# Kernel tuning notes

Measured on AMD Instinct MI355X. Metric: run time of the kernel, lower is better.

## Reference

```python
import jax, jax.numpy as jnp
import numpy as np

B, CIN, T, H, W = 4, 3, 32, 64, 64
COUT = 64


def setup_inputs() -> dict:
    key = jax.random.key(0)
    ks = jax.random.split(key, 6)
    X = jax.random.normal(ks[0], (B, CIN, T, H, W), jnp.float32)
    # Conv3d weight (O, I, D, kH, kW) for kernel (2,3,3)
    Wconv = jax.random.normal(ks[1], (4 * COUT, CIN, 2, 3, 3), jnp.float32) * 0.1
    bconv = jax.random.normal(ks[2], (4 * COUT,), jnp.float32) * 0.1
    # QRNNCell peephole params, shape (out_channels, *frame_size)
    W_ci = jax.random.normal(ks[3], (COUT, H, W), jnp.float32) * 0.1
    W_cf = jax.random.normal(ks[4], (COUT, H, W), jnp.float32) * 0.1
    W_co = jax.random.normal(ks[5], (COUT, H, W), jnp.float32) * 0.1
    return {"X": X, "Wconv": Wconv, "bconv": bconv,
            "W_ci": W_ci, "W_cf": W_cf, "W_co": W_co}


def reference(X, Wconv, bconv, W_ci, W_cf, W_co):
    # ConstantPad3d((1,1,1,1,1,0)): W +-1, H +-1, time front +1
    Xp = jnp.pad(X, ((0, 0), (0, 0), (1, 0), (1, 1), (1, 1)))
    # Conv3d, kernel (2,3,3), VALID -> output (B, 4*COUT, T, H, W)
    E = jax.lax.conv_general_dilated(
        Xp, Wconv, window_strides=(1, 1, 1), padding='VALID',
        dimension_numbers=('NCDHW', 'OIDHW', 'NCDHW'))
    E = E + bconv[None, :, None, None, None]
    i_c, f_c, g_c, o_c = jnp.split(E, 4, axis=1)  # each (B, COUT, T, H, W)
    # time-major stacked gates: (T, 4, B, COUT, H, W)
    gates = jnp.stack([jnp.moveaxis(x, 2, 0) for x in (i_c, f_c, g_c, o_c)], axis=1)

    def step(carry, g4):
        Hs, Cs = carry
        i, f, g, o = g4[0], g4[1], g4[2], g4[3]
        ig = jax.nn.sigmoid(i + W_ci * Cs)
        fg = jax.nn.sigmoid(f + W_cf * Cs)
        Cn = fg * Cs + ig * jnp.tanh(g)
        og = jax.nn.sigmoid(o + W_co * Cn)
        Hn = og * jnp.tanh(Cn)
        return (Hn, Cn), Hn

    z = jnp.zeros((X.shape[0], W_ci.shape[0], X.shape[3], X.shape[4]), X.dtype)
    _, outs = jax.lax.scan(step, (z, z), gates)  # outs: (T, B, COUT, H, W)
    return jnp.moveaxis(outs, 0, 2)  # (B, COUT, T, H, W)
```

## Files before the change

kernel.cpp:

```cpp
#include <hip/hip_runtime.h>

#define TT     32
#define HW     4096
#define LROW   68
#define LPLANE (6 * LROW)
#define SXSZ   (3 * LPLANE)
#define NSTG   (3 * 6 * 66)

__device__ __forceinline__ float fsigmoid(float x) {
    return __builtin_amdgcn_rcpf(1.0f + __builtin_amdgcn_exp2f(x * -1.4426950408889634f));
}
__device__ __forceinline__ float ftanh(float x) {
    return 2.0f * __builtin_amdgcn_rcpf(1.0f + __builtin_amdgcn_exp2f(x * -2.8853900817779268f)) - 1.0f;
}
__device__ __forceinline__ float sgprf(float v) {
    return __uint_as_float(__builtin_amdgcn_readfirstlane(__float_as_uint(v)));
}

__global__ __launch_bounds__(256, 2) void convqrnn(
    const float* __restrict__ X,
    const float* __restrict__ Wc,
    const float* __restrict__ bc,
    const float* __restrict__ Wci,
    const float* __restrict__ Wcf,
    const float* __restrict__ Wco,
    float* __restrict__ out)
{
    __shared__ float sx[2 * SXSZ];
    __shared__ float gb[2 * 2048];
    __shared__ float wl[576];

    const int tid = threadIdx.x;
    const int h0  = blockIdx.x * 4;
    const int co0 = blockIdx.y * 2;
    const int b   = blockIdx.z;

    const int g  = tid >> 6;
    const int l  = tid & 63;
    const int r  = l >> 4;
    const int c0 = (l & 15) * 4;

    const int prow = tid >> 6;
    const int pcol = tid & 63;
    const int opix = (h0 + prow) * 64 + pcol;

    const float wciA = Wci[co0 * HW + opix];
    const float wcfA = Wcf[co0 * HW + opix];
    const float wcoA = Wco[co0 * HW + opix];
    const float wciB = Wci[(co0 + 1) * HW + opix];
    const float wcfB = Wcf[(co0 + 1) * HW + opix];
    const float wcoB = Wco[(co0 + 1) * HW + opix];

    for (int fi = tid; fi < 432; fi += 256) {
        int grp   = fi / 12;
        int e     = fi - grp * 12;
        int g2    = grp / 9;
        int ck    = grp - g2 * 9;
        int ci    = ck / 3;
        int kh    = ck - ci * 3;
        int which = e / 3;
        int kw    = e - which * 3;
        int cs    = which >> 1;
        int dt    = which & 1;
        wl[grp * 16 + e] =
            Wc[(size_t)(g2 * 64 + co0 + cs) * 54 + ci * 18 + dt * 9 + kh * 3 + kw];
    }
    const float bgA = sgprf(bc[g * 64 + co0]);
    const float bgB = sgprf(bc[g * 64 + co0 + 1]);

    const float* __restrict__ Xb = X + (size_t)b * (3 * TT * HW);
    int soff[5];
    int goff[5];
    int svmask = 0;
    #pragma unroll
    for (int k = 0; k < 5; ++k) {
        int idx  = tid + k * 256;
        bool inr = (idx < NSTG);
        int idc  = inr ? idx : 0;
        int ci   = idc / 396;
        int rem  = idc - ci * 396;
        int y    = rem / 66;
        int x    = rem - y * 66;
        int gh   = h0 + y - 1;
        int gw   = x - 1;
        bool v   = inr && (gh >= 0) && (gh < 64) && (gw >= 0) && (gw < 64);
        int ghc  = gh < 0 ? 0 : (gh > 63 ? 63 : gh);
        int gwc  = gw < 0 ? 0 : (gw > 63 ? 63 : gw);
        soff[k]  = inr ? (ci * LPLANE + y * LROW + x) : (LROW - 1);
        goff[k]  = ci * (TT * HW) + ghc * 64 + gwc;
        svmask  |= (v ? 1 : 0) << k;
    }

    #pragma unroll
    for (int k = 0; k < 5; ++k) {
        float v = ((svmask >> k) & 1) ? Xb[goff[k]] : 0.0f;
        sx[soff[k]] = v;
        goff[k] += HW;
    }

    float* __restrict__ outA = out + (size_t)(b * 64 + co0) * (TT * HW);
    float* __restrict__ outB = outA + (size_t)(TT * HW);
    int ooff = opix;

    float aA0 = 0.f, aA1 = 0.f, aA2 = 0.f, aA3 = 0.f;
    float aB0 = 0.f, aB1 = 0.f, aB2 = 0.f, aB3 = 0.f;
    float CA = 0.f, CB = 0.f;

    __syncthreads();

    for (int t = 0; t < TT; ++t) {
        if (blockIdx.x == 0xFFFFFFFFu) wl[tid] = 0.0f;

        const float* __restrict__ sxb = &sx[(t & 1) * SXSZ];
        float*       __restrict__ gbb = &gb[(t & 1) * 2048];

        float stv[5];
        if (t < TT - 1) {
            #pragma unroll
            for (int k = 0; k < 5; ++k) {
                stv[k] = ((svmask >> k) & 1) ? Xb[goff[k]] : 0.0f;
                goff[k] += HW;
            }
        }

        float sA0 = bgA, sA1 = bgA, sA2 = bgA, sA3 = bgA;
        float sB0 = bgB, sB1 = bgB, sB2 = bgB, sB3 = bgB;
        float nA0 = 0.f, nA1 = 0.f, nA2 = 0.f, nA3 = 0.f;
        float nB0 = 0.f, nB1 = 0.f, nB2 = 0.f, nB3 = 0.f;
        #pragma unroll
        for (int ci = 0; ci < 3; ++ci)
            #pragma unroll
            for (int kh = 0; kh < 3; ++kh) {
                const float* rowp = &sxb[ci * LPLANE + (r + kh) * LROW + c0];
                float4 lo = *(const float4*)rowp;
                float2 hi = *(const float2*)(rowp + 4);
                const float w0 = lo.x, w1 = lo.y, w2 = lo.z;
                const float w3 = lo.w, w4 = hi.x, w5 = hi.y;

                const int ws = (g * 9 + ci * 3 + kh) * 16;
                float4 qa = *(const float4*)&wl[ws];
                float4 qb = *(const float4*)&wl[ws + 4];
                float4 qc = *(const float4*)&wl[ws + 8];

                sA0 += qa.w * w0;  sA1 += qa.w * w1;  sA2 += qa.w * w2;  sA3 += qa.w * w3;
                sA0 += qb.x * w1;  sA1 += qb.x * w2;  sA2 += qb.x * w3;  sA3 += qb.x * w4;
                sA0 += qb.y * w2;  sA1 += qb.y * w3;  sA2 += qb.y * w4;  sA3 += qb.y * w5;

                nA0 += qa.x * w0;  nA1 += qa.x * w1;  nA2 += qa.x * w2;  nA3 += qa.x * w3;
                nA0 += qa.y * w1;  nA1 += qa.y * w2;  nA2 += qa.y * w3;  nA3 += qa.y * w4;
                nA0 += qa.z * w2;  nA1 += qa.z * w3;  nA2 += qa.z * w4;  nA3 += qa.z * w5;

                sB0 += qc.y * w0;  sB1 += qc.y * w1;  sB2 += qc.y * w2;  sB3 += qc.y * w3;
                sB0 += qc.z * w1;  sB1 += qc.z * w2;  sB2 += qc.z * w3;  sB3 += qc.z * w4;
                sB0 += qc.w * w2;  sB1 += qc.w * w3;  sB2 += qc.w * w4;  sB3 += qc.w * w5;

                nB0 += qb.z * w0;  nB1 += qb.z * w1;  nB2 += qb.z * w2;  nB3 += qb.z * w3;
                nB0 += qb.w * w1;  nB1 += qb.w * w2;  nB2 += qb.w * w3;  nB3 += qb.w * w4;
                nB0 += qc.x * w2;  nB1 += qc.x * w3;  nB2 += qc.x * w4;  nB3 += qc.x * w5;
            }

        float4 gvA = make_float4(sA0 + aA0, sA1 + aA1, sA2 + aA2, sA3 + aA3);
        float4 gvB = make_float4(sB0 + aB0, sB1 + aB1, sB2 + aB2, sB3 + aB3);
        aA0 = nA0; aA1 = nA1; aA2 = nA2; aA3 = nA3;
        aB0 = nB0; aB1 = nB1; aB2 = nB2; aB3 = nB3;
        *(float4*)&gbb[g * 256 + r * 64 + c0]        = gvA;
        *(float4*)&gbb[1024 + g * 256 + r * 64 + c0] = gvB;

        if (t < TT - 1) {
            float* __restrict__ sxn = &sx[((t + 1) & 1) * SXSZ];
            #pragma unroll
            for (int k = 0; k < 5; ++k) sxn[soff[k]] = stv[k];
        }

        __syncthreads();

        {
            const float iv = gbb[tid];
            const float fv = gbb[256 + tid];
            const float gg = gbb[512 + tid];
            const float ov = gbb[768 + tid];
            const float ig = fsigmoid(iv + wciA * CA);
            const float fg = fsigmoid(fv + wcfA * CA);
            const float Cn = fg * CA + ig * ftanh(gg);
            const float og = fsigmoid(ov + wcoA * Cn);
            outA[ooff] = og * ftanh(Cn);
            CA = Cn;
        }
        {
            const float iv = gbb[1024 + tid];
            const float fv = gbb[1024 + 256 + tid];
            const float gg = gbb[1024 + 512 + tid];
            const float ov = gbb[1024 + 768 + tid];
            const float ig = fsigmoid(iv + wciB * CB);
            const float fg = fsigmoid(fv + wcfB * CB);
            const float Cn = fg * CB + ig * ftanh(gg);
            const float og = fsigmoid(ov + wcoB * Cn);
            outB[ooff] = og * ftanh(Cn);
            CB = Cn;
        }
        ooff += HW;
    }
}

extern "C" void kernel_launch(void* const* d_in, const int* in_sizes, int n_in,
                              void* d_out, int out_size, void* d_ws, size_t ws_size,
                              hipStream_t stream) {
    const float* X   = (const float*)d_in[0];
    const float* Wc  = (const float*)d_in[1];
    const float* bc  = (const float*)d_in[2];
    const float* Wci = (const float*)d_in[3];
    const float* Wcf = (const float*)d_in[4];
    const float* Wco = (const float*)d_in[5];
    float* out = (float*)d_out;

    dim3 grid(16, 32, 4);
    convqrnn<<<grid, 256, 0, stream>>>(X, Wc, bc, Wci, Wcf, Wco, out);
}
```

Baseline: 377.5 us.

## Software-pipeline conv of next timestep with recurrent update of current step

Restructures the time loop so the convolution for step t+1 is computed before the gate/cell update of step t. Two input planes are prefetched up front, and the X prefetch runs two steps ahead. The goal is to let the independent conv FMAs and the latency-bound sigmoid/tanh recurrence interleave within one barrier interval, cutting the number of serialized phases per step. The cost is an extra prologue conv, a deeper prefetch, and more live registers.

```diff
diff --git a/kernel.cpp b/kernel.cpp
--- a/kernel.cpp
+++ b/kernel.cpp
@@ -97,6 +97,12 @@
         sx[soff[k]] = v;
         goff[k] += HW;
     }
+    #pragma unroll
+    for (int k = 0; k < 5; ++k) {
+        float v = ((svmask >> k) & 1) ? Xb[goff[k]] : 0.0f;
+        sx[SXSZ + soff[k]] = v;
+        goff[k] += HW;
+    }
 
     float* __restrict__ outA = out + (size_t)(b * 64 + co0) * (TT * HW);
     float* __restrict__ outB = outA + (size_t)(TT * HW);
@@ -106,25 +112,9 @@
     float aB0 = 0.f, aB1 = 0.f, aB2 = 0.f, aB3 = 0.f;
     float CA = 0.f, CB = 0.f;
 
-    __syncthreads();
-
-    for (int t = 0; t < TT; ++t) {
-        if (blockIdx.x == 0xFFFFFFFFu) wl[tid] = 0.0f;
-
-        const float* __restrict__ sxb = &sx[(t & 1) * SXSZ];
-        float*       __restrict__ gbb = &gb[(t & 1) * 2048];
-
-        float stv[5];
-        if (t < TT - 1) {
-            #pragma unroll
-            for (int k = 0; k < 5; ++k) {
-                stv[k] = ((svmask >> k) & 1) ? Xb[goff[k]] : 0.0f;
-                goff[k] += HW;
-            }
-        }
-
-        float sA0 = bgA, sA1 = bgA, sA2 = bgA, sA3 = bgA;
-        float sB0 = bgB, sB1 = bgB, sB2 = bgB, sB3 = bgB;
+    auto conv_and_post = [&](const float* sxb, float* gbb) {
+        float sA0 = bgA + aA0, sA1 = bgA + aA1, sA2 = bgA + aA2, sA3 = bgA + aA3;
+        float sB0 = bgB + aB0, sB1 = bgB + aB1, sB2 = bgB + aB2, sB3 = bgB + aB3;
         float nA0 = 0.f, nA1 = 0.f, nA2 = 0.f, nA3 = 0.f;
         float nB0 = 0.f, nB1 = 0.f, nB2 = 0.f, nB3 = 0.f;
         #pragma unroll
@@ -158,47 +148,72 @@
                 nB0 += qb.w * w1;  nB1 += qb.w * w2;  nB2 += qb.w * w3;  nB3 += qb.w * w4;
                 nB0 += qc.x * w2;  nB1 += qc.x * w3;  nB2 += qc.x * w4;  nB3 += qc.x * w5;
             }
-
-        float4 gvA = make_float4(sA0 + aA0, sA1 + aA1, sA2 + aA2, sA3 + aA3);
-        float4 gvB = make_float4(sB0 + aB0, sB1 + aB1, sB2 + aB2, sB3 + aB3);
         aA0 = nA0; aA1 = nA1; aA2 = nA2; aA3 = nA3;
         aB0 = nB0; aB1 = nB1; aB2 = nB2; aB3 = nB3;
-        *(float4*)&gbb[g * 256 + r * 64 + c0]        = gvA;
-        *(float4*)&gbb[1024 + g * 256 + r * 64 + c0] = gvB;
-
-        if (t < TT - 1) {
-            float* __restrict__ sxn = &sx[((t + 1) & 1) * SXSZ];
+        *(float4*)&gbb[g * 256 + r * 64 + c0]        = make_float4(sA0, sA1, sA2, sA3);
+        *(float4*)&gbb[1024 + g * 256 + r * 64 + c0] = make_float4(sB0, sB1, sB2, sB3);
+    };
+
+    __syncthreads();
+
+    conv_and_post(&sx[0], &gb[0]);
+
+    __syncthreads();
+
+    for (int t = 0; t < TT; ++t) {
+        if (blockIdx.x == 0xFFFFFFFFu) wl[tid] = 0.0f;
+
+        const bool haveNext   = (t < TT - 1);
+        const bool havePlane2 = (t < TT - 2);
+
+        float stv[5];
+        if (havePlane2) {
+            #pragma unroll
+            for (int k = 0; k < 5; ++k) {
+                stv[k] = ((svmask >> k) & 1) ? Xb[goff[k]] : 0.0f;
+                goff[k] += HW;
+            }
+        }
+
+        if (haveNext)
+            conv_and_post(&sx[((t + 1) & 1) * SXSZ], &gb[((t + 1) & 1) * 2048]);
+
+        {
+            const float* gbb = &gb[(t & 1) * 2048];
+            {
+                const float iv = gbb[tid];
+                const float fv = gbb[256 + tid];
+                const float gg = gbb[512 + tid];
+                const float ov = gbb[768 + tid];
+                const float ig = fsigmoid(iv + wciA * CA);
+                const float fg = fsigmoid(fv + wcfA * CA);
+                const float Cn = fg * CA + ig * ftanh(gg);
+                const float og = fsigmoid(ov + wcoA * Cn);
+                outA[ooff] = og * ftanh(Cn);
+                CA = Cn;
+            }
+            {
+                const float iv = gbb[1024 + tid];
+                const float fv = gbb[1024 + 256 + tid];
+                const float gg = gbb[1024 + 512 + tid];
+                const float ov = gbb[1024 + 768 + tid];
+                const float ig = fsigmoid(iv + wciB * CB);
+                const float fg = fsigmoid(fv + wcfB * CB);
+                const float Cn = fg * CB + ig * ftanh(gg);
+                const float og = fsigmoid(ov + wcoB * Cn);
+                outB[ooff] = og * ftanh(Cn);
+                CB = Cn;
+            }
+            ooff += HW;
+        }
+
+        if (havePlane2) {
+            float* __restrict__ sxn = &sx[(t & 1) * SXSZ];
             #pragma unroll
             for (int k = 0; k < 5; ++k) sxn[soff[k]] = stv[k];
         }
 
         __syncthreads();
-
-        {
-            const float iv = gbb[tid];
-            const float fv = gbb[256 + tid];
-            const float gg = gbb[512 + tid];
-            const float ov = gbb[768 + tid];
-            const float ig = fsigmoid(iv + wciA * CA);
-            const float fg = fsigmoid(fv + wcfA * CA);
-            const float Cn = fg * CA + ig * ftanh(gg);
-            const float og = fsigmoid(ov + wcoA * Cn);
-            outA[ooff] = og * ftanh(Cn);
-            CA = Cn;
-        }
-        {
-            const float iv = gbb[1024 + tid];
-            const float fv = gbb[1024 + 256 + tid];
-            const float gg = gbb[1024 + 512 + tid];
-            const float ov = gbb[1024 + 768 + tid];
-            const float ig = fsigmoid(iv + wciB * CB);
-            const float fg = fsigmoid(fv + wcfB * CB);
-            const float Cn = fg * CB + ig * ftanh(gg);
-            const float og = fsigmoid(ov + wcoB * Cn);
-            outB[ooff] = og * ftanh(Cn);
-            CB = Cn;
-        }
-        ooff += HW;
     }
 }
 
```

Result: slower. 457.3 us (+21.1%).
